# Performance work log

Hardware: AMD Instinct MI355X
Metric: run time of the kernel (lower is better)

The kernel has to match this reference:

```python
import jax, jax.numpy as jnp
import numpy as np

B, E, S, H = 4, 1024, 1024, 16
HD = E // H  # head_size = 64
MASK_VALUE = -1000000000.0
W_SCALE = 0.05  # keep pre-softmax logits moderate since original softmax is not max-stabilized


def setup_inputs() -> dict:
    key = jax.random.key(0)
    ks = jax.random.split(key, 7)
    queries = jax.random.normal(ks[0], (B, E, S), jnp.float32)
    keys = jax.random.normal(ks[1], (B, E, S), jnp.float32)
    values = jax.random.normal(ks[2], (B, E, S), jnp.float32)
    # causal multiplicative mask, broadcast over batch
    mask = jnp.broadcast_to(jnp.tril(jnp.ones((S, S), jnp.float32)), (B, S, S))
    Wq = jax.random.normal(ks[3], (H, HD, HD), jnp.float32) * W_SCALE
    Wk = jax.random.normal(ks[4], (H, HD, HD), jnp.float32) * W_SCALE
    Wv = jax.random.normal(ks[5], (H, HD, HD), jnp.float32) * W_SCALE
    Wf = jax.random.normal(ks[6], (E, E), jnp.float32) * W_SCALE
    return dict(queries=queries, keys=keys, values=values, mask=mask,
                Wq=Wq, Wk=Wk, Wv=Wv, Wf=Wf)


def reference(queries, keys, values, mask, Wq, Wk, Wv, Wf):
    # channels-first: [B, E, S] -> split embedding axis into heads: [B, H, HD, S]
    qh = queries.reshape(B, H, HD, S)
    kh = keys.reshape(B, H, HD, S)
    vh = values.reshape(B, H, HD, S)
    # per-head linear projections: W[h] @ x_slice, batched over heads
    q = jnp.einsum('hde,bhes->bhds', Wq, qh)
    k = jnp.einsum('hde,bhes->bhds', Wk, kh)
    v = jnp.einsum('hde,bhes->bhds', Wv, vh)
    # pre_softmax = Q^T @ K / sqrt(head_size)  -> [B, H, S, S]
    pre = jnp.einsum('bhds,bhdt->bhst', q, k) / jnp.sqrt(jnp.float32(HD))
    m = mask[:, None, :, :]  # broadcast mask over heads
    pre = pre * m + (m == 0).astype(jnp.float32) * MASK_VALUE
    # Faithful to original: exp / reduce_sum(axis=-1)[..., None, :]
    # i.e. post[b,h,i,j] = exp(pre[b,h,i,j]) / sum_t exp(pre[b,h,j,t])
    e = jnp.exp(pre)
    post = e / jnp.sum(e, axis=3)[:, :, None, :]
    # values @ post^T : out[b,h,d,i] = sum_j v[b,h,d,j] * post[b,h,i,j]
    out_h = jnp.einsum('bhdj,bhij->bhdi', v, post)
    pre_linear = out_h.reshape(B, E, S)  # concat heads along embedding axis
    return jnp.einsum('ef,bfs->bes', Wf, pre_linear)
```

## Files before the change

### kernel.cpp

```cpp
#include <hip/hip_runtime.h>
#include <hip/hip_bf16.h>
#include <stdint.h>

#define NB 4
#define NH 16
#define HDIM 64
#define NS 1024
#define NE 1024

typedef __bf16 bf16x8 __attribute__((ext_vector_type(8)));
typedef __bf16 bf16x2_t __attribute__((ext_vector_type(2)));
typedef float f32x4 __attribute__((ext_vector_type(4)));
typedef float f32x16 __attribute__((ext_vector_type(16)));
typedef unsigned int uint4v __attribute__((ext_vector_type(4)));
typedef unsigned int uint2v __attribute__((ext_vector_type(2)));
typedef unsigned short u16;

#if defined(__has_builtin)
#if __has_builtin(__builtin_amdgcn_global_load_lds)
#define HAVE_GLDS 1
#endif
#endif

__device__ __forceinline__ u16 f2bf(float f) {
  return __builtin_bit_cast(u16, (__bf16)f);
}
__device__ __forceinline__ unsigned pk2(float a, float b) {
  bf16x2_t v; v[0] = (__bf16)a; v[1] = (__bf16)b;
  return __builtin_bit_cast(unsigned, v);
}
__device__ __forceinline__ float fexp2(float x) {
#if defined(__has_builtin)
#if __has_builtin(__builtin_amdgcn_exp2f)
  return __builtin_amdgcn_exp2f(x);
#else
  return __expf(x * 0.69314718056f);
#endif
#else
  return __expf(x * 0.69314718056f);
#endif
}
__device__ __forceinline__ f32x4 mfma16(bf16x8 a, bf16x8 b, f32x4 c) {
  return __builtin_amdgcn_mfma_f32_16x16x32_bf16(a, b, c, 0, 0, 0);
}
__device__ __forceinline__ f32x16 mfma32(bf16x8 a, bf16x8 b, f32x16 c) {
  return __builtin_amdgcn_mfma_f32_32x32x16_bf16(a, b, c, 0, 0, 0);
}
__device__ __forceinline__ bf16x8 ld_bf8(const u16* p) {
  return __builtin_bit_cast(bf16x8, *(const uint4v*)p);
}
#ifdef HAVE_GLDS
__device__ __forceinline__ void gld16(const void* g, void* l) {
  __builtin_amdgcn_global_load_lds(
      (__attribute__((address_space(1))) void*)g,
      (__attribute__((address_space(3))) void*)l, 16, 0, 0);
}
#endif

#if defined(__has_builtin)
#if __has_builtin(__builtin_amdgcn_permlane32_swap)
#define HAVE_PLS 1
#endif
#endif
__device__ __forceinline__ uint2v plswap(unsigned a, unsigned b) {
#ifdef HAVE_PLS
  return __builtin_amdgcn_permlane32_swap(a, b, false, false);
#else
  unsigned asw = (unsigned)__shfl_xor((int)a, 32);
  unsigned bsw = (unsigned)__shfl_xor((int)b, 32);
  bool hi = (threadIdx.x & 32) != 0;
  uint2v r;
  r[0] = hi ? bsw : a;
  r[1] = hi ? b : asw;
  return r;
#endif
}

__global__ __launch_bounds__(256) void proj_kernel(
    const float* __restrict__ q_in, const float* __restrict__ k_in,
    const float* __restrict__ v_in, const float* __restrict__ Wq,
    const float* __restrict__ Wk, const float* __restrict__ Wv,
    const float* __restrict__ Wf,
    u16* __restrict__ qT, u16* __restrict__ kT, u16* __restrict__ vv,
    u16* __restrict__ Wf16)
{
  const int which = blockIdx.z;
  const int tid = threadIdx.x;

  if (which == 3) {
    int chunk = blockIdx.y * 4 + blockIdx.x;
    #pragma unroll
    for (int jj = 0; jj < 4; ++jj) {
      int i = chunk * 1024 + tid + 256 * jj;
      float4 f = ((const float4*)Wf)[i];
      uint2v p;
      p[0] = pk2(f.x, f.y);
      p[1] = pk2(f.z, f.w);
      ((uint2v*)Wf16)[i] = p;
    }
    return;
  }

  const int bh = blockIdx.y;
  const int b = bh >> 4, h = bh & 15;
  const int s0 = blockIdx.x * 256;
  const int w = tid >> 6, l = tid & 63, lr = l & 15, lg = l >> 4;

  const float* x = (which == 0) ? q_in : (which == 1) ? k_in : v_in;
  const float* W = ((which == 0) ? Wq : (which == 1) ? Wk : Wv) + h * 4096;
  const float wsc = (which == 0) ? 0.18033688f : 1.0f;

  __shared__ alignas(16) u16 xT[256][72];
  __shared__ alignas(16) u16 Wl[64][72];

  #pragma unroll
  for (int j = 0; j < 4; ++j) {
    int i = tid * 4 + j;
    int d = i >> 4;
    int e0 = (i & 15) * 4;
    float4 f = *(const float4*)(W + d * 64 + e0);
    uint2v p;
    p[0] = pk2(f.x * wsc, f.y * wsc);
    p[1] = pk2(f.z * wsc, f.w * wsc);
    *(uint2v*)&Wl[d][e0] = p;
  }
  {
    const float* xp = x + ((size_t)b * NE + h * 64) * NS + s0 + tid;
    #pragma unroll
    for (int j = 0; j < 8; ++j) {
      uint4v pk;
      #pragma unroll
      for (int q = 0; q < 4; ++q) {
        float f0 = xp[(size_t)(j * 8 + q * 2) * NS];
        float f1 = xp[(size_t)(j * 8 + q * 2 + 1) * NS];
        pk[q] = pk2(f0, f1);
      }
      *(uint4v*)&xT[tid][j * 8] = pk;
    }
  }
  __syncthreads();

  bf16x8 af[4][2];
  #pragma unroll
  for (int mt = 0; mt < 4; ++mt) {
    af[mt][0] = ld_bf8(&Wl[mt * 16 + lr][lg * 8]);
    af[mt][1] = ld_bf8(&Wl[mt * 16 + lr][32 + lg * 8]);
  }
  f32x4 acc[4][4] = {};
  #pragma unroll
  for (int nt = 0; nt < 4; ++nt) {
    bf16x8 b0 = ld_bf8(&xT[w * 64 + nt * 16 + lr][lg * 8]);
    bf16x8 b1 = ld_bf8(&xT[w * 64 + nt * 16 + lr][32 + lg * 8]);
    #pragma unroll
    for (int mt = 0; mt < 4; ++mt) {
      acc[mt][nt] = mfma16(af[mt][0], b0, acc[mt][nt]);
      acc[mt][nt] = mfma16(af[mt][1], b1, acc[mt][nt]);
    }
  }

  if (which < 2) {
    u16* o = ((which == 0) ? qT : kT) + (size_t)bh * NS * 64;
    #pragma unroll
    for (int mt = 0; mt < 4; ++mt)
      #pragma unroll
      for (int nt = 0; nt < 4; ++nt) {
        int s = s0 + w * 64 + nt * 16 + lr;
        int d = mt * 16 + lg * 4;
        uint2v p;
        p[0] = pk2(acc[mt][nt][0], acc[mt][nt][1]);
        p[1] = pk2(acc[mt][nt][2], acc[mt][nt][3]);
        *(uint2v*)(o + (size_t)s * 64 + d) = p;
      }
  } else {
    u16* o = vv + (size_t)bh * 64 * NS;
    #pragma unroll
    for (int mt = 0; mt < 4; ++mt)
      #pragma unroll
      for (int nt = 0; nt < 4; ++nt)
        #pragma unroll
        for (int jr = 0; jr < 4; ++jr) {
          int d = mt * 16 + lg * 4 + jr;
          int s = s0 + w * 64 + nt * 16 + lr;
          o[(size_t)d * NS + s] = f2bf(acc[mt][nt][jr]);
        }
  }
}

__global__ __launch_bounds__(256) void denom_kernel(
    const u16* __restrict__ qT, const u16* __restrict__ kT,
    float* __restrict__ l2rDg)
{
  const int wg = blockIdx.x;
  const int rt = 7 - (wg >> 6);
  const int bh = wg & 63;
  const int i0 = rt * 128;
  const int tid = threadIdx.x, w = tid >> 6, l = tid & 63;
  const int q5 = l & 31, hf = l >> 5;
  __shared__ alignas(16) u16 klds[128][72];
  const u16* qb = qT + (size_t)bh * NS * 64;
  const u16* kb = kT + (size_t)bh * NS * 64;
  const int r0w = i0 + w * 32;
  const int gi2 = r0w + q5;
  bf16x8 bq[4];
  #pragma unroll
  for (int dc = 0; dc < 4; ++dc)
    bq[dc] = ld_bf8(qb + (size_t)gi2 * 64 + dc * 16 + hf * 8);
  float den = 0.f;
  const int nkt = rt + 1;
  uint4v kreg[4];
  const int krow = tid >> 3, kcx = tid & 7;
  #pragma unroll
  for (int j = 0; j < 4; ++j)
    kreg[j] = *(const uint4v*)(kb + (size_t)(krow + j * 32) * 64 + kcx * 8);
  for (int t = 0; t < nkt; ++t) {
    __syncthreads();
    #pragma unroll
    for (int j = 0; j < 4; ++j)
      *(uint4v*)&klds[krow + j * 32][kcx * 8] = kreg[j];
    __syncthreads();
    const int t0 = t * 128;
    if (t + 1 < nkt) {
      #pragma unroll
      for (int j = 0; j < 4; ++j)
        kreg[j] = *(const uint4v*)(kb + (size_t)(t0 + 128 + krow + j * 32) * 64 + kcx * 8);
    }
    #pragma unroll
    for (int kbi = 0; kbi < 4; ++kbi) {
      const int kb0 = t0 + kbi * 32;
      if (kb0 > r0w + 31) continue;
      const bool msk = (kb0 + 31 > r0w);
      f32x16 sc = {};
      #pragma unroll
      for (int dc = 0; dc < 4; ++dc) {
        bf16x8 ak = ld_bf8(&klds[kbi * 32 + q5][dc * 16 + hf * 8]);
        sc = mfma32(ak, bq[dc], sc);
      }
      if (!msk) {
        #pragma unroll
        for (int r = 0; r < 16; ++r) den += fexp2(sc[r]);
      } else {
        #pragma unroll
        for (int r = 0; r < 16; ++r) {
          int key = kb0 + (r & 3) + 8 * (r >> 2) + 4 * hf;
          den += (key <= gi2) ? fexp2(sc[r]) : 0.f;
        }
      }
    }
  }
  den += __shfl_xor(den, 32);
  if (l < 32) l2rDg[(size_t)bh * NS + gi2] = -__log2f(den);
}

__global__ __launch_bounds__(256) void attn_kernel(
    const u16* __restrict__ qT, const u16* __restrict__ kT,
    const u16* __restrict__ vv, const float* __restrict__ l2rDg,
    u16* __restrict__ X)
{
  const int wg = blockIdx.x;
  const int rt = 7 - (wg >> 6);
  const int bh = wg & 63;
  const int b = bh >> 4, h = bh & 15;
  const int i0 = rt * 128;
  const int tid = threadIdx.x, w = tid >> 6, l = tid & 63;
  const int q5 = l & 31, hf = l >> 5;
  __shared__ alignas(16) u16 klds[64][72];
  __shared__ alignas(16) u16 vlds[64][72];
  __shared__ alignas(16) float dlds[64];
  const u16* qb = qT + (size_t)bh * NS * 64;
  const u16* kb = kT + (size_t)bh * NS * 64;
  const u16* vb = vv + (size_t)bh * 64 * NS;
  const float* rb = l2rDg + (size_t)bh * NS;
  const int r0w = i0 + w * 32;
  const int gi2 = r0w + q5;
  bf16x8 bq[4];
  #pragma unroll
  for (int dc = 0; dc < 4; ++dc)
    bq[dc] = ld_bf8(qb + (size_t)gi2 * 64 + dc * 16 + hf * 8);
  f32x16 acc[2] = {};
  const int nkt = 2 * rt + 2;
  uint4v kreg[2], vreg[2];
  float dreg = 0.f;
  const int krow = tid >> 3, kcx = tid & 7;
  #pragma unroll
  for (int j = 0; j < 2; ++j) {
    kreg[j] = *(const uint4v*)(kb + (size_t)(krow + j * 32) * 64 + kcx * 8);
    vreg[j] = *(const uint4v*)(vb + (size_t)(krow + j * 32) * NS + kcx * 8);
  }
  if (tid < 64) dreg = rb[tid];
  for (int t = 0; t < nkt; ++t) {
    __syncthreads();
    #pragma unroll
    for (int j = 0; j < 2; ++j) {
      *(uint4v*)&klds[krow + j * 32][kcx * 8] = kreg[j];
      *(uint4v*)&vlds[krow + j * 32][kcx * 8] = vreg[j];
    }
    if (tid < 64) dlds[tid] = dreg;
    __syncthreads();
    const int t0 = t * 64;
    if (t + 1 < nkt) {
      const int t0n = t0 + 64;
      #pragma unroll
      for (int j = 0; j < 2; ++j) {
        kreg[j] = *(const uint4v*)(kb + (size_t)(t0n + krow + j * 32) * 64 + kcx * 8);
        vreg[j] = *(const uint4v*)(vb + (size_t)(krow + j * 32) * NS + t0n + kcx * 8);
      }
      if (tid < 64) dreg = rb[t0n + tid];
    }
    #pragma unroll
    for (int kbi = 0; kbi < 2; ++kbi) {
      const int kb0 = t0 + kbi * 32;
      if (kb0 > r0w + 31) continue;
      const bool msk = (kb0 + 31 > r0w);
      f32x16 sc = {};
      #pragma unroll
      for (int dc = 0; dc < 4; ++dc) {
        bf16x8 ak = ld_bf8(&klds[kbi * 32 + q5][dc * 16 + hf * 8]);
        sc = mfma32(ak, bq[dc], sc);
      }
      f32x4 lv[4];
      #pragma unroll
      for (int g = 0; g < 4; ++g)
        lv[g] = *(const f32x4*)&dlds[kbi * 32 + 4 * hf + 8 * g];
      float p[16];
      if (!msk) {
        #pragma unroll
        for (int r = 0; r < 16; ++r)
          p[r] = fexp2(sc[r] + lv[r >> 2][r & 3]);
      } else {
        #pragma unroll
        for (int r = 0; r < 16; ++r) {
          int key = kb0 + (r & 3) + 8 * (r >> 2) + 4 * hf;
          float e = fexp2(sc[r] + lv[r >> 2][r & 3]);
          p[r] = (key <= gi2) ? e : 0.f;
        }
      }
      bf16x8 pa[2];
      #pragma unroll
      for (int f = 0; f < 2; ++f) {
        unsigned A0 = pk2(p[8 * f + 0], p[8 * f + 1]);
        unsigned A1 = pk2(p[8 * f + 2], p[8 * f + 3]);
        unsigned B0 = pk2(p[8 * f + 4], p[8 * f + 5]);
        unsigned B1 = pk2(p[8 * f + 6], p[8 * f + 7]);
        uint2v s0 = plswap(A0, B0);
        uint2v s1 = plswap(A1, B1);
        uint4v fw;
        fw[0] = s0[0]; fw[1] = s1[0]; fw[2] = s0[1]; fw[3] = s1[1];
        pa[f] = __builtin_bit_cast(bf16x8, fw);
      }
      __builtin_amdgcn_s_setprio(1);
      #pragma unroll
      for (int db = 0; db < 2; ++db) {
        #pragma unroll
        for (int f = 0; f < 2; ++f) {
          bf16x8 bv = ld_bf8(&vlds[db * 32 + q5][kbi * 32 + f * 16 + hf * 8]);
          acc[db] = mfma32(pa[f], bv, acc[db]);
        }
      }
      __builtin_amdgcn_s_setprio(0);
    }
  }
  u16* Xp = X + (size_t)b * NS * NE + h * 64;
  #pragma unroll
  for (int db = 0; db < 2; ++db)
    #pragma unroll
    for (int r = 0; r < 16; ++r) {
      int srow = r0w + (r & 3) + 8 * (r >> 2) + 4 * hf;
      Xp[(size_t)srow * NE + db * 32 + q5] = f2bf(acc[db][r]);
    }
}

__global__ __launch_bounds__(256) void final_gemm(
    const u16* __restrict__ Wf16, const u16* __restrict__ X,
    float* __restrict__ out)
{
  const int b = blockIdx.z;
  const int e0 = blockIdx.y * 128;
  const int s0 = blockIdx.x * 128;
  const int tid = threadIdx.x, w = tid >> 6, l = tid & 63, lr = l & 15, lg = l >> 4;
  const int wm = (w >> 1) * 64, wn = (w & 1) * 64;
  __shared__ alignas(16) u16 Ald[2][128][64];
  __shared__ alignas(16) u16 Bld[2][128][64];
  const u16* Xb = X + (size_t)b * NS * NE;
  f32x4 acc[4][4] = {};

  #define FG_ISSUE(p, k0)                                                     \
    {                                                                         \
      _Pragma("unroll")                                                       \
      for (int j = 0; j < 4; ++j) {                                           \
        int c = tid + 256 * j;                                                \
        int r = c >> 3;                                                       \
        int sc_ = ((c & 7) * 16) ^ ((r & 7) << 4);                            \
        const char* ga = (const char*)(Wf16 + (size_t)(e0 + r) * NE + (k0)) + sc_; \
        const char* gb = (const char*)(Xb + (size_t)(s0 + r) * NE + (k0)) + sc_;   \
        char* la = (char*)&Ald[p][0][0] + c * 16;                             \
        char* lb = (char*)&Bld[p][0][0] + c * 16;                             \
        STAGE16(ga, la);                                                      \
        STAGE16(gb, lb);                                                      \
      }                                                                       \
    }
#ifdef HAVE_GLDS
  #define STAGE16(g, l_) gld16((g), (l_))
#else
  #define STAGE16(g, l_) (*(uint4v*)(l_) = *(const uint4v*)(g))
#endif

  FG_ISSUE(0, 0);
  __syncthreads();
  for (int t = 0; t < 16; ++t) {
    const int p = t & 1;
    if (t < 15) FG_ISSUE(p ^ 1, (t + 1) * 64);
    __builtin_amdgcn_s_setprio(1);
    #pragma unroll
    for (int kk = 0; kk < 2; ++kk) {
      bf16x8 a[4], bb[4];
      #pragma unroll
      for (int mt = 0; mt < 4; ++mt) {
        int R = wm + mt * 16 + lr;
        a[mt] = ld_bf8((const u16*)((const char*)&Ald[p][R][0] +
                                    ((kk * 64 + lg * 16) ^ ((R & 7) << 4))));
      }
      #pragma unroll
      for (int nt = 0; nt < 4; ++nt) {
        int R = wn + nt * 16 + lr;
        bb[nt] = ld_bf8((const u16*)((const char*)&Bld[p][R][0] +
                                     ((kk * 64 + lg * 16) ^ ((R & 7) << 4))));
      }
      #pragma unroll
      for (int mt = 0; mt < 4; ++mt)
        #pragma unroll
        for (int nt = 0; nt < 4; ++nt)
          acc[mt][nt] = mfma16(a[mt], bb[nt], acc[mt][nt]);
    }
    __builtin_amdgcn_s_setprio(0);
    __syncthreads();
  }
  #pragma unroll
  for (int mt = 0; mt < 4; ++mt)
    #pragma unroll
    for (int nt = 0; nt < 4; ++nt) {
      int e = e0 + wm + mt * 16 + lg * 4;
      int s = s0 + wn + nt * 16 + lr;
      float* op = out + ((size_t)b * NE + e) * NS + s;
      op[0] = acc[mt][nt][0];
      op[NS] = acc[mt][nt][1];
      op[2 * NS] = acc[mt][nt][2];
      op[3 * NS] = acc[mt][nt][3];
    }
}

extern "C" void kernel_launch(void* const* d_in, const int* in_sizes, int n_in,
                              void* d_out, int out_size, void* d_ws, size_t ws_size,
                              hipStream_t stream) {
  (void)in_sizes; (void)n_in; (void)out_size; (void)ws_size;
  const float* q_in = (const float*)d_in[0];
  const float* k_in = (const float*)d_in[1];
  const float* v_in = (const float*)d_in[2];
  const float* Wq = (const float*)d_in[4];
  const float* Wk = (const float*)d_in[5];
  const float* Wv = (const float*)d_in[6];
  const float* Wf = (const float*)d_in[7];

  u16* qT = (u16*)d_ws;
  u16* kT = qT + (size_t)NB * NH * NS * HDIM;
  u16* vv = kT + (size_t)NB * NH * NS * HDIM;
  u16* X  = vv + (size_t)NB * NH * HDIM * NS;
  u16* Wf16 = X + (size_t)NB * NS * NE;
  float* l2rD = (float*)(Wf16 + (size_t)NE * NE);

  proj_kernel<<<dim3(4, 64, 4), 256, 0, stream>>>(q_in, k_in, v_in, Wq, Wk, Wv,
                                                  Wf, qT, kT, vv, Wf16);
  denom_kernel<<<dim3(512), 256, 0, stream>>>(qT, kT, l2rD);
  attn_kernel<<<dim3(512), 256, 0, stream>>>(qT, kT, vv, l2rD, X);
  final_gemm<<<dim3(8, 8, 4), 256, 0, stream>>>(Wf16, X, (float*)d_out);
}
```

Baseline: 79.16 us.

## Rebalance work splits across denom, attention and final GEMM kernels

The denominator kernel moves to 512 threads using 16x16 MFMA tiles, with one wave per 16 query rows. The attention kernel now uses 64-row query tiles, split into two key halves across wave pairs with an LDS reduction at the end, and double-buffers its K/V/denominator tiles to save one barrier per step. The final GEMM moves to 512 threads with narrower per-wave tiles. The aim is more parallelism and occupancy and less per-block imbalance on the causal triangle. The cost is more blocks, an extra cross-wave reduction and more register and LDS pressure.

```diff
diff --git a/kernel.cpp b/kernel.cpp
--- a/kernel.cpp
+++ b/kernel.cpp
@@ -186,7 +186,7 @@
   }
 }
 
-__global__ __launch_bounds__(256) void denom_kernel(
+__global__ __launch_bounds__(512) void denom_kernel(
     const u16* __restrict__ qT, const u16* __restrict__ kT,
     float* __restrict__ l2rDg)
 {
@@ -194,61 +194,61 @@
   const int rt = 7 - (wg >> 6);
   const int bh = wg & 63;
   const int i0 = rt * 128;
-  const int tid = threadIdx.x, w = tid >> 6, l = tid & 63;
-  const int q5 = l & 31, hf = l >> 5;
+  const int tid = threadIdx.x, w = tid >> 6, l = tid & 63, lr = l & 15, lg = l >> 4;
   __shared__ alignas(16) u16 klds[128][72];
   const u16* qb = qT + (size_t)bh * NS * 64;
   const u16* kb = kT + (size_t)bh * NS * 64;
-  const int r0w = i0 + w * 32;
-  const int gi2 = r0w + q5;
-  bf16x8 bq[4];
-  #pragma unroll
-  for (int dc = 0; dc < 4; ++dc)
-    bq[dc] = ld_bf8(qb + (size_t)gi2 * 64 + dc * 16 + hf * 8);
+  const int gi = i0 + w * 16 + lr;
+  bf16x8 bq0 = ld_bf8(qb + (size_t)gi * 64 + lg * 8);
+  bf16x8 bq1 = ld_bf8(qb + (size_t)gi * 64 + 32 + lg * 8);
   float den = 0.f;
   const int nkt = rt + 1;
-  uint4v kreg[4];
+  uint4v kreg[2];
   const int krow = tid >> 3, kcx = tid & 7;
   #pragma unroll
-  for (int j = 0; j < 4; ++j)
-    kreg[j] = *(const uint4v*)(kb + (size_t)(krow + j * 32) * 64 + kcx * 8);
+  for (int j = 0; j < 2; ++j)
+    kreg[j] = *(const uint4v*)(kb + (size_t)(krow + j * 64) * 64 + kcx * 8);
   for (int t = 0; t < nkt; ++t) {
     __syncthreads();
     #pragma unroll
-    for (int j = 0; j < 4; ++j)
-      *(uint4v*)&klds[krow + j * 32][kcx * 8] = kreg[j];
+    for (int j = 0; j < 2; ++j)
+      *(uint4v*)&klds[krow + j * 64][kcx * 8] = kreg[j];
     __syncthreads();
     const int t0 = t * 128;
     if (t + 1 < nkt) {
       #pragma unroll
-      for (int j = 0; j < 4; ++j)
-        kreg[j] = *(const uint4v*)(kb + (size_t)(t0 + 128 + krow + j * 32) * 64 + kcx * 8);
-    }
-    #pragma unroll
-    for (int kbi = 0; kbi < 4; ++kbi) {
-      const int kb0 = t0 + kbi * 32;
-      if (kb0 > r0w + 31) continue;
-      const bool msk = (kb0 + 31 > r0w);
-      f32x16 sc = {};
-      #pragma unroll
-      for (int dc = 0; dc < 4; ++dc) {
-        bf16x8 ak = ld_bf8(&klds[kbi * 32 + q5][dc * 16 + hf * 8]);
-        sc = mfma32(ak, bq[dc], sc);
-      }
-      if (!msk) {
+      for (int j = 0; j < 2; ++j)
+        kreg[j] = *(const uint4v*)(kb + (size_t)(t0 + 128 + krow + j * 64) * 64 + kcx * 8);
+    }
+    if (t + 1 < nkt) {
+      #pragma unroll
+      for (int mt = 0; mt < 8; ++mt) {
+        bf16x8 a0 = ld_bf8(&klds[mt * 16 + lr][lg * 8]);
+        bf16x8 a1 = ld_bf8(&klds[mt * 16 + lr][32 + lg * 8]);
+        f32x4 z = {0.f, 0.f, 0.f, 0.f};
+        f32x4 sc = mfma16(a0, bq0, z);
+        sc = mfma16(a1, bq1, sc);
+        den += fexp2(sc[0]) + fexp2(sc[1]) + fexp2(sc[2]) + fexp2(sc[3]);
+      }
+    } else {
+      #pragma unroll
+      for (int mt = 0; mt < 8; ++mt) {
+        bf16x8 a0 = ld_bf8(&klds[mt * 16 + lr][lg * 8]);
+        bf16x8 a1 = ld_bf8(&klds[mt * 16 + lr][32 + lg * 8]);
+        f32x4 z = {0.f, 0.f, 0.f, 0.f};
+        f32x4 sc = mfma16(a0, bq0, z);
+        sc = mfma16(a1, bq1, sc);
         #pragma unroll
-        for (int r = 0; r < 16; ++r) den += fexp2(sc[r]);
-      } else {
-        #pragma unroll
-        for (int r = 0; r < 16; ++r) {
-          int key = kb0 + (r & 3) + 8 * (r >> 2) + 4 * hf;
-          den += (key <= gi2) ? fexp2(sc[r]) : 0.f;
+        for (int r = 0; r < 4; ++r) {
+          int gt = t0 + mt * 16 + lg * 4 + r;
+          den += (gt <= gi) ? fexp2(sc[r]) : 0.f;
         }
       }
     }
   }
+  den += __shfl_xor(den, 16);
   den += __shfl_xor(den, 32);
-  if (l < 32) l2rDg[(size_t)bh * NS + gi2] = -__log2f(den);
+  if (l < 16) l2rDg[(size_t)bh * NS + gi] = -__log2f(den);
 }
 
 __global__ __launch_bounds__(256) void attn_kernel(
@@ -257,90 +257,94 @@
     u16* __restrict__ X)
 {
   const int wg = blockIdx.x;
-  const int rt = 7 - (wg >> 6);
+  const int rt = 15 - (wg >> 6);
   const int bh = wg & 63;
   const int b = bh >> 4, h = bh & 15;
-  const int i0 = rt * 128;
+  const int i0 = rt * 64;
   const int tid = threadIdx.x, w = tid >> 6, l = tid & 63;
   const int q5 = l & 31, hf = l >> 5;
-  __shared__ alignas(16) u16 klds[64][72];
-  __shared__ alignas(16) u16 vlds[64][72];
-  __shared__ alignas(16) float dlds[64];
+  const int qi = w >> 1, ki = w & 1;
+
+  __shared__ alignas(16) unsigned char smem[2 * 64 * 72 * 2 * 2 + 2 * 64 * 4];
+  typedef u16 (*tile_t)[64][72];
+  tile_t klds = (tile_t)smem;
+  tile_t vlds = (tile_t)(smem + 18432);
+  float (*dlds)[64] = (float(*)[64])(smem + 36864);
+
   const u16* qb = qT + (size_t)bh * NS * 64;
   const u16* kb = kT + (size_t)bh * NS * 64;
   const u16* vb = vv + (size_t)bh * 64 * NS;
   const float* rb = l2rDg + (size_t)bh * NS;
-  const int r0w = i0 + w * 32;
+  const int r0w = i0 + qi * 32;
   const int gi2 = r0w + q5;
   bf16x8 bq[4];
   #pragma unroll
   for (int dc = 0; dc < 4; ++dc)
     bq[dc] = ld_bf8(qb + (size_t)gi2 * 64 + dc * 16 + hf * 8);
   f32x16 acc[2] = {};
-  const int nkt = 2 * rt + 2;
+  const int nkt = rt + 1;
   uint4v kreg[2], vreg[2];
   float dreg = 0.f;
-  const int krow = tid >> 3, kcx = tid & 7;
+  const int crow = tid >> 3, ccx = tid & 7;
   #pragma unroll
   for (int j = 0; j < 2; ++j) {
-    kreg[j] = *(const uint4v*)(kb + (size_t)(krow + j * 32) * 64 + kcx * 8);
-    vreg[j] = *(const uint4v*)(vb + (size_t)(krow + j * 32) * NS + kcx * 8);
+    kreg[j] = *(const uint4v*)(kb + (size_t)(crow + j * 32) * 64 + ccx * 8);
+    vreg[j] = *(const uint4v*)(vb + (size_t)(crow + j * 32) * NS + ccx * 8);
   }
   if (tid < 64) dreg = rb[tid];
+  #pragma unroll
+  for (int j = 0; j < 2; ++j) {
+    *(uint4v*)&klds[0][crow + j * 32][ccx * 8] = kreg[j];
+    *(uint4v*)&vlds[0][crow + j * 32][ccx * 8] = vreg[j];
+  }
+  if (tid < 64) dlds[0][tid] = dreg;
+  __syncthreads();
+  int p = 0;
   for (int t = 0; t < nkt; ++t) {
-    __syncthreads();
-    #pragma unroll
-    for (int j = 0; j < 2; ++j) {
-      *(uint4v*)&klds[krow + j * 32][kcx * 8] = kreg[j];
-      *(uint4v*)&vlds[krow + j * 32][kcx * 8] = vreg[j];
-    }
-    if (tid < 64) dlds[tid] = dreg;
-    __syncthreads();
     const int t0 = t * 64;
-    if (t + 1 < nkt) {
+    const bool more = (t + 1 < nkt);
+    if (more) {
       const int t0n = t0 + 64;
       #pragma unroll
       for (int j = 0; j < 2; ++j) {
-        kreg[j] = *(const uint4v*)(kb + (size_t)(t0n + krow + j * 32) * 64 + kcx * 8);
-        vreg[j] = *(const uint4v*)(vb + (size_t)(krow + j * 32) * NS + t0n + kcx * 8);
+        kreg[j] = *(const uint4v*)(kb + (size_t)(t0n + crow + j * 32) * 64 + ccx * 8);
+        vreg[j] = *(const uint4v*)(vb + (size_t)(crow + j * 32) * NS + t0n + ccx * 8);
       }
       if (tid < 64) dreg = rb[t0n + tid];
     }
-    #pragma unroll
-    for (int kbi = 0; kbi < 2; ++kbi) {
-      const int kb0 = t0 + kbi * 32;
-      if (kb0 > r0w + 31) continue;
+    const int kb0 = t0 + ki * 32;
+    if (kb0 <= r0w + 31) {
       const bool msk = (kb0 + 31 > r0w);
       f32x16 sc = {};
       #pragma unroll
       for (int dc = 0; dc < 4; ++dc) {
-        bf16x8 ak = ld_bf8(&klds[kbi * 32 + q5][dc * 16 + hf * 8]);
+        bf16x8 ak = ld_bf8(&klds[p][ki * 32 + q5][dc * 16 + hf * 8]);
         sc = mfma32(ak, bq[dc], sc);
       }
       f32x4 lv[4];
       #pragma unroll
       for (int g = 0; g < 4; ++g)
-        lv[g] = *(const f32x4*)&dlds[kbi * 32 + 4 * hf + 8 * g];
-      float p[16];
+        lv[g] = *(const f32x4*)&dlds[p][ki * 32 + 4 * hf + 8 * g];
+      float pe[16];
       if (!msk) {
         #pragma unroll
         for (int r = 0; r < 16; ++r)
-          p[r] = fexp2(sc[r] + lv[r >> 2][r & 3]);
+          pe[r] = fexp2(sc[r] + lv[r >> 2][r & 3]);
       } else {
         #pragma unroll
         for (int r = 0; r < 16; ++r) {
           int key = kb0 + (r & 3) + 8 * (r >> 2) + 4 * hf;
           float e = fexp2(sc[r] + lv[r >> 2][r & 3]);
-          p[r] = (key <= gi2) ? e : 0.f;
+          pe[r] = (key <= gi2) ? e : 0.f;
         }
       }
       bf16x8 pa[2];
       #pragma unroll
       for (int f = 0; f < 2; ++f) {
-        unsigned A0 = pk2(p[8 * f + 0], p[8 * f + 1]);
-        unsigned A1 = pk2(p[8 * f + 2], p[8 * f + 3]);
-        unsigned B0 = pk2(p[8 * f + 4], p[8 * f + 5]);
-        unsigned B1 = pk2(p[8 * f + 6], p[8 * f + 7]);
+        unsigned A0 = pk2(pe[8 * f + 0], pe[8 * f + 1]);
+        unsigned A1 = pk2(pe[8 * f + 2], pe[8 * f + 3]);
+        unsigned B0 = pk2(pe[8 * f + 4], pe[8 * f + 5]);
+        unsigned B1 = pk2(pe[8 * f + 6], pe[8 * f + 7]);
         uint2v s0 = plswap(A0, B0);
         uint2v s1 = plswap(A1, B1);
         uint4v fw;
@@ -352,24 +356,50 @@
       for (int db = 0; db < 2; ++db) {
         #pragma unroll
         for (int f = 0; f < 2; ++f) {
-          bf16x8 bv = ld_bf8(&vlds[db * 32 + q5][kbi * 32 + f * 16 + hf * 8]);
+          bf16x8 bv = ld_bf8(&vlds[p][db * 32 + q5][ki * 32 + f * 16 + hf * 8]);
           acc[db] = mfma32(pa[f], bv, acc[db]);
         }
       }
       __builtin_amdgcn_s_setprio(0);
     }
-  }
-  u16* Xp = X + (size_t)b * NS * NE + h * 64;
-  #pragma unroll
-  for (int db = 0; db < 2; ++db)
-    #pragma unroll
-    for (int r = 0; r < 16; ++r) {
-      int srow = r0w + (r & 3) + 8 * (r >> 2) + 4 * hf;
-      Xp[(size_t)srow * NE + db * 32 + q5] = f2bf(acc[db][r]);
-    }
-}
-
-__global__ __launch_bounds__(256) void final_gemm(
+    if (more) {
+      #pragma unroll
+      for (int j = 0; j < 2; ++j) {
+        *(uint4v*)&klds[p ^ 1][crow + j * 32][ccx * 8] = kreg[j];
+        *(uint4v*)&vlds[p ^ 1][crow + j * 32][ccx * 8] = vreg[j];
+      }
+      if (tid < 64) dlds[p ^ 1][tid] = dreg;
+      __syncthreads();
+      p ^= 1;
+    }
+  }
+  __syncthreads();
+  float* flds = (float*)smem;
+  if (ki == 1) {
+    #pragma unroll
+    for (int db = 0; db < 2; ++db)
+      #pragma unroll
+      for (int r = 0; r < 16; ++r) {
+        int qrow = (r & 3) + 8 * (r >> 2) + 4 * hf;
+        flds[(qi * 32 + qrow) * 64 + db * 32 + q5] = acc[db][r];
+      }
+  }
+  __syncthreads();
+  if (ki == 0) {
+    u16* Xp = X + (size_t)b * NS * NE + h * 64;
+    #pragma unroll
+    for (int db = 0; db < 2; ++db)
+      #pragma unroll
+      for (int r = 0; r < 16; ++r) {
+        int qrow = (r & 3) + 8 * (r >> 2) + 4 * hf;
+        float v = acc[db][r] + flds[(qi * 32 + qrow) * 64 + db * 32 + q5];
+        int srow = r0w + qrow;
+        Xp[(size_t)srow * NE + db * 32 + q5] = f2bf(v);
+      }
+  }
+}
+
+__global__ __launch_bounds__(512) void final_gemm(
     const u16* __restrict__ Wf16, const u16* __restrict__ X,
     float* __restrict__ out)
 {
@@ -377,17 +407,17 @@
   const int e0 = blockIdx.y * 128;
   const int s0 = blockIdx.x * 128;
   const int tid = threadIdx.x, w = tid >> 6, l = tid & 63, lr = l & 15, lg = l >> 4;
-  const int wm = (w >> 1) * 64, wn = (w & 1) * 64;
+  const int wm = (w >> 2) * 64, wn = (w & 3) * 32;
   __shared__ alignas(16) u16 Ald[2][128][64];
   __shared__ alignas(16) u16 Bld[2][128][64];
   const u16* Xb = X + (size_t)b * NS * NE;
-  f32x4 acc[4][4] = {};
+  f32x4 acc[4][2] = {};
 
   #define FG_ISSUE(p, k0)                                                     \
     {                                                                         \
       _Pragma("unroll")                                                       \
-      for (int j = 0; j < 4; ++j) {                                           \
-        int c = tid + 256 * j;                                                \
+      for (int j = 0; j < 2; ++j) {                                           \
+        int c = tid + 512 * j;                                                \
         int r = c >> 3;                                                       \
         int sc_ = ((c & 7) * 16) ^ ((r & 7) << 4);                            \
         const char* ga = (const char*)(Wf16 + (size_t)(e0 + r) * NE + (k0)) + sc_; \
@@ -412,7 +442,7 @@
     __builtin_amdgcn_s_setprio(1);
     #pragma unroll
     for (int kk = 0; kk < 2; ++kk) {
-      bf16x8 a[4], bb[4];
+      bf16x8 a[4], bb[2];
       #pragma unroll
       for (int mt = 0; mt < 4; ++mt) {
         int R = wm + mt * 16 + lr;
@@ -420,7 +450,7 @@
                                     ((kk * 64 + lg * 16) ^ ((R & 7) << 4))));
       }
       #pragma unroll
-      for (int nt = 0; nt < 4; ++nt) {
+      for (int nt = 0; nt < 2; ++nt) {
         int R = wn + nt * 16 + lr;
         bb[nt] = ld_bf8((const u16*)((const char*)&Bld[p][R][0] +
                                      ((kk * 64 + lg * 16) ^ ((R & 7) << 4))));
@@ -428,7 +458,7 @@
       #pragma unroll
       for (int mt = 0; mt < 4; ++mt)
         #pragma unroll
-        for (int nt = 0; nt < 4; ++nt)
+        for (int nt = 0; nt < 2; ++nt)
           acc[mt][nt] = mfma16(a[mt], bb[nt], acc[mt][nt]);
     }
     __builtin_amdgcn_s_setprio(0);
@@ -437,7 +467,7 @@
   #pragma unroll
   for (int mt = 0; mt < 4; ++mt)
     #pragma unroll
-    for (int nt = 0; nt < 4; ++nt) {
+    for (int nt = 0; nt < 2; ++nt) {
       int e = e0 + wm + mt * 16 + lg * 4;
       int s = s0 + wn + nt * 16 + lr;
       float* op = out + ((size_t)b * NE + e) * NS + s;
@@ -469,7 +499,7 @@
 
   proj_kernel<<<dim3(4, 64, 4), 256, 0, stream>>>(q_in, k_in, v_in, Wq, Wk, Wv,
                                                   Wf, qT, kT, vv, Wf16);
-  denom_kernel<<<dim3(512), 256, 0, stream>>>(qT, kT, l2rD);
-  attn_kernel<<<dim3(512), 256, 0, stream>>>(qT, kT, vv, l2rD, X);
-  final_gemm<<<dim3(8, 8, 4), 256, 0, stream>>>(Wf16, X, (float*)d_out);
-}
+  denom_kernel<<<dim3(512), 512, 0, stream>>>(qT, kT, l2rD);
+  attn_kernel<<<dim3(1024), 256, 0, stream>>>(qT, kT, vv, l2rD, X);
+  final_gemm<<<dim3(8, 8, 4), 512, 0, stream>>>(Wf16, X, (float*)d_out);
+}
```

Measured after the change: 70.77 us, median of 2. 1.12x faster.
